# Performance work log

Measured on AMD Instinct MI355X. Metric: run time of the kernel, lower is better.

Reference implementation:

```python
import jax, jax.numpy as jnp
import numpy as np

B, S, D, H = 2, 1024, 768, 12
HD = D // H          # head_dim = 64
DFF = 4 * D          # 3072
EPS = 1e-5


def _ln(x, g, b):
    m = x.mean(-1, keepdims=True)
    v = ((x - m) ** 2).mean(-1, keepdims=True)
    return (x - m) * jax.lax.rsqrt(v + EPS) * g + b


def setup_inputs() -> dict:
    key = jax.random.key(0)
    ks = jax.random.split(key, 8)
    w = lambda k, shape: jax.random.normal(k, shape, jnp.float32) * 0.02
    return {
        "inp": jax.random.normal(ks[0], (B, S, D), jnp.float32),
        "attention_mask": jnp.zeros((B, S), bool),  # True = masked out (filled with -inf)
        "rel_matrix": jax.random.randint(ks[1], (B, S, S), -1, 2, jnp.int32),  # values in {-1,0,1}
        "qkv_w": w(ks[2], (3 * D, D)),
        "rel_A": w(ks[3], (3, HD)),        # relative_position_emb_A.weight
        "o_w": w(ks[4], (D, D)),
        "w1": w(ks[5], (DFF, D)), "b1": jnp.zeros((DFF,), jnp.float32),
        "w2": w(ks[6], (D, DFF)), "b2": jnp.zeros((D,), jnp.float32),
        "ln1_g": jnp.ones((D,), jnp.float32), "ln1_b": jnp.zeros((D,), jnp.float32),
        "ln2_g": jnp.ones((D,), jnp.float32), "ln2_b": jnp.zeros((D,), jnp.float32),
    }


def reference(inp, attention_mask, rel_matrix, qkv_w, rel_A, o_w,
              w1, b1, w2, b2, ln1_g, ln1_b, ln2_g, ln2_b):
    x = _ln(inp, ln1_g, ln1_b)
    qkv = x @ qkv_w.T                                  # (B,S,3D)
    q, k, v = jnp.split(qkv, 3, axis=-1)
    heads = lambda t: t.reshape(B, S, H, HD).transpose(0, 2, 1, 3)  # (B,H,S,HD)
    q, k, v = heads(q), heads(k), heads(v)

    # q @ (k + rel_emb)^T without materializing k_aug:
    # q.k^T term plus per-(q,key) relative term gathered from q @ A^T.
    logits = jnp.einsum("bhqd,bhkd->bhqk", q, k)       # (B,H,S,S)
    r = jnp.einsum("bhqd,cd->bhqc", q, rel_A)          # (B,H,S,3)
    idx = (rel_matrix + 1).astype(jnp.int32)           # (B,S,S) in {0,1,2}
    rel = jnp.take_along_axis(r, jnp.broadcast_to(idx[:, None], (B, H, S, S)), axis=-1)
    logits = (logits + rel) / np.sqrt(HD).astype(np.float32)
    # masked_fill: -inf where mask is True
    logits = jnp.where(attention_mask[:, None, None, :], -jnp.inf, logits)

    attn = jax.nn.softmax(logits, axis=-1)
    out = jnp.einsum("bhqk,bhkd->bhqd", attn, v)
    out = out.transpose(0, 2, 1, 3).reshape(B, S, D)
    inp = inp + out @ o_w.T                            # residual (dropout=0)

    h = _ln(inp, ln2_g, ln2_b)
    mlp = jax.nn.relu(h @ w1.T + b1) @ w2.T + b2
    return inp + mlp
```

## Files before the change

kernel.cpp:

```cpp
#include <hip/hip_runtime.h>
#include <hip/hip_bf16.h>

#define BB 2
#define SS 1024
#define DD 768
#define HH 12
#define HD 64
#define DFF 3072
#define EPS 1e-5f
#define BS2 (BB * SS)
#define BSD ((size_t)BS2 * DD)

typedef unsigned short ushort_t;
typedef unsigned char uchar_t;
using short8 = __attribute__((ext_vector_type(8))) short;
using f32x4  = __attribute__((ext_vector_type(4))) float;

__device__ __forceinline__ ushort_t f2bf_rne(float f) {
    union { float f; unsigned u; } x; x.f = f;
    unsigned r = x.u + 0x7fff + ((x.u >> 16) & 1);
    return (ushort_t)(r >> 16);
}
__device__ __forceinline__ float bf2f(short u) {
    union { unsigned i; float f; } x;
    x.i = ((unsigned)(ushort_t)u) << 16;
    return x.f;
}

#define CVT_N1 (3 * DD * DD / 4)
#define CVT_N2 (CVT_N1 + DD * DD / 4)
#define CVT_N3 (CVT_N2 + DFF * DD / 4)
#define CVT_NT (CVT_N3 + DD * DFF / 4)
#define PREP_CVT   (CVT_NT / 256)
#define PREP_CODES (BB * SS)
#define PREP_LN    BS2

__global__ __launch_bounds__(256) void prep_kernel(
    const float* __restrict__ qkv_w, const float* __restrict__ o_w,
    const float* __restrict__ w1, const float* __restrict__ w2,
    ushort_t* __restrict__ wdst,
    const int* __restrict__ rel, const uchar_t* __restrict__ mask,
    unsigned* __restrict__ codes,
    const float* __restrict__ x, const float* __restrict__ g,
    const float* __restrict__ b, ushort_t* __restrict__ y)
{
    const int bx = blockIdx.x;
    const int t  = threadIdx.x;
    if (bx < PREP_CVT) {
        int i = bx * 256 + t;
        const float* src; int off;
        if (i < CVT_N1)      { src = qkv_w; off = i; }
        else if (i < CVT_N2) { src = o_w;   off = i - CVT_N1; }
        else if (i < CVT_N3) { src = w1;    off = i - CVT_N2; }
        else                 { src = w2;    off = i - CVT_N3; }
        float4 v = ((const float4*)src)[off];
        ushort4 o;
        o.x = f2bf_rne(v.x); o.y = f2bf_rne(v.y);
        o.z = f2bf_rne(v.z); o.w = f2bf_rne(v.w);
        ((ushort4*)wdst)[i] = o;
        return;
    }
    if (bx < PREP_CVT + PREP_CODES) {
        int tid = (bx - PREP_CVT) * 256 + t;
        int l15 = tid & 15;
        int kt  = (tid >> 4) & 15;
        int q   = (tid >> 8) & (SS - 1);
        int bb  = tid >> 18;
        const int* rrow = rel + ((size_t)(bb * SS + q)) * SS + kt * 64 + l15;
        const uchar_t* mrow = mask + (size_t)bb * SS + kt * 64 + l15;
        unsigned o = 0;
#pragma unroll
        for (int nt = 0; nt < 4; ++nt) {
            unsigned c = mrow[nt * 16] ? 3u : (unsigned)(rrow[nt * 16] + 1);
            o |= c << (8 * nt);
        }
        codes[((size_t)(bb * SS + q) * 16 + kt) * 16 + l15] = o;
        return;
    }
    const int row = bx - PREP_CVT - PREP_CODES;
    const float* xr = x + (size_t)row * DD;
    float s = 0.f, ss = 0.f;
    for (int i = t; i < DD; i += 256) {
        float v = xr[i];
        s += v; ss += v * v;
    }
    for (int off = 32; off; off >>= 1) {
        s  += __shfl_down(s,  off);
        ss += __shfl_down(ss, off);
    }
    __shared__ float reds[4], redss[4], bc[2];
    if ((t & 63) == 0) { reds[t >> 6] = s; redss[t >> 6] = ss; }
    __syncthreads();
    if (t == 0) {
        float S1 = reds[0] + reds[1] + reds[2] + reds[3];
        float S2 = redss[0] + redss[1] + redss[2] + redss[3];
        float mean = S1 / DD;
        float var = S2 / DD - mean * mean;
        bc[0] = mean;
        bc[1] = rsqrtf(var + EPS);
    }
    __syncthreads();
    float mean = bc[0], inv = bc[1];
    ushort_t* yr = y + (size_t)row * DD;
    for (int i = t; i < DD; i += 256) {
        yr[i] = f2bf_rne((xr[i] - mean) * inv * g[i] + b[i]);
    }
}

__global__ __launch_bounds__(256) void merge2_ln_kernel(
    const float* __restrict__ part, const float* __restrict__ inp,
    const float* __restrict__ g, const float* __restrict__ b,
    float* __restrict__ resid, ushort_t* __restrict__ h_bf)
{
    const int row = blockIdx.x;
    const int t = threadIdx.x;
    float4 v = make_float4(0.f, 0.f, 0.f, 0.f);
    const size_t idx = (size_t)row * (DD / 4) + t;
    if (t < DD / 4) {
        v = ((const float4*)inp)[idx];
        float4 p0 = ((const float4*)part)[idx];
        float4 p1 = ((const float4*)(part + BSD))[idx];
        v.x += p0.x + p1.x; v.y += p0.y + p1.y;
        v.z += p0.z + p1.z; v.w += p0.w + p1.w;
        ((float4*)resid)[idx] = v;
    }
    float s  = v.x + v.y + v.z + v.w;
    float ss = v.x * v.x + v.y * v.y + v.z * v.z + v.w * v.w;
    for (int off = 32; off; off >>= 1) {
        s  += __shfl_down(s,  off);
        ss += __shfl_down(ss, off);
    }
    __shared__ float reds[4], redss[4], bc[2];
    if ((t & 63) == 0) { reds[t >> 6] = s; redss[t >> 6] = ss; }
    __syncthreads();
    if (t == 0) {
        float S1 = reds[0] + reds[1] + reds[2] + reds[3];
        float S2 = redss[0] + redss[1] + redss[2] + redss[3];
        float mean = S1 / DD;
        float var = S2 / DD - mean * mean;
        bc[0] = mean;
        bc[1] = rsqrtf(var + EPS);
    }
    __syncthreads();
    if (t < DD / 4) {
        const float mean = bc[0], inv = bc[1];
        float4 gv = ((const float4*)g)[t];
        float4 bv = ((const float4*)b)[t];
        ushort4 o;
        o.x = f2bf_rne((v.x - mean) * inv * gv.x + bv.x);
        o.y = f2bf_rne((v.y - mean) * inv * gv.y + bv.y);
        o.z = f2bf_rne((v.z - mean) * inv * gv.z + bv.z);
        o.w = f2bf_rne((v.w - mean) * inv * gv.w + bv.w);
        ((ushort4*)h_bf)[idx] = o;
    }
}

__global__ __launch_bounds__(256) void merge4_kernel(
    const float* __restrict__ part, const float* __restrict__ resid,
    const float* __restrict__ b2, float* __restrict__ outp, int n4)
{
    int i = blockIdx.x * 256 + threadIdx.x;
    if (i >= n4) return;
    float4 v = ((const float4*)resid)[i];
    int col4 = (i * 4) % DD;
    float4 bv = *(const float4*)(b2 + col4);
    v.x += bv.x; v.y += bv.y; v.z += bv.z; v.w += bv.w;
#pragma unroll
    for (int z = 0; z < 4; ++z) {
        float4 pz = ((const float4*)(part + (size_t)z * BSD))[i];
        v.x += pz.x; v.y += pz.y; v.z += pz.z; v.w += pz.w;
    }
    ((float4*)outp)[i] = v;
}

template <bool RELU, bool OUT_BF16, bool HAS_BIAS, bool PARTIAL>
__global__ __launch_bounds__(256) void gemm_tile(
    const ushort_t* __restrict__ A, const ushort_t* __restrict__ W,
    const float* __restrict__ bias, void* __restrict__ Cout,
    int M, int N, int K, int Ksplit)
{
    __shared__ __align__(16) ushort_t As[512 * 8];
    __shared__ __align__(16) ushort_t Bs[1024 * 8];

    const int t  = threadIdx.x;
    const int n0 = blockIdx.x * 128;
    const int m0 = blockIdx.y * 64;
    const int kb = blockIdx.z * Ksplit;
    const int w  = t >> 6;
    const int l  = t & 63;
    const int wm = (w & 1) * 32;
    const int wn = (w >> 1) * 64;
    const int l15  = l & 15;
    const int quad = l >> 4;

    const ushort_t* gA = A + (size_t)(m0 + (t & 63)) * K + kb + (t >> 6) * 8;
    ushort_t* lA = &As[(size_t)t * 8];
    const ushort_t* gB = W + (size_t)(n0 + (t & 127)) * K + kb + (t >> 7) * 8;
    ushort_t* lB = &Bs[(size_t)t * 8];

    f32x4 acc[2][4] = {};

    for (int k0 = 0; k0 < Ksplit; k0 += 64) {
        __syncthreads();
        __builtin_amdgcn_global_load_lds(
            (const __attribute__((address_space(1))) unsigned int*)(gA + k0),
            (__attribute__((address_space(3))) unsigned int*)lA, 16, 0, 0);
        __builtin_amdgcn_global_load_lds(
            (const __attribute__((address_space(1))) unsigned int*)(gA + k0 + 32),
            (__attribute__((address_space(3))) unsigned int*)(lA + 256 * 8), 16, 0, 0);
#pragma unroll
        for (int ii = 0; ii < 4; ++ii)
            __builtin_amdgcn_global_load_lds(
                (const __attribute__((address_space(1))) unsigned int*)(gB + k0 + ii * 16),
                (__attribute__((address_space(3))) unsigned int*)(lB + (size_t)ii * 256 * 8),
                16, 0, 0);
        __syncthreads();

#pragma unroll
        for (int ks = 0; ks < 2; ++ks) {
            const ushort_t* aptr = &As[(size_t)((ks * 4 + quad) * 64 + wm + l15) * 8];
            const ushort_t* bptr = &Bs[(size_t)((ks * 4 + quad) * 128 + wn + l15) * 8];
            short8 af[2], bf[4];
#pragma unroll
            for (int i = 0; i < 2; ++i)
                af[i] = *(const short8*)(aptr + (size_t)i * 16 * 8);
#pragma unroll
            for (int j = 0; j < 4; ++j)
                bf[j] = *(const short8*)(bptr + (size_t)j * 16 * 8);
#pragma unroll
            for (int i = 0; i < 2; ++i)
#pragma unroll
                for (int j = 0; j < 4; ++j)
                    acc[i][j] = __builtin_amdgcn_mfma_f32_16x16x32_bf16(
                        af[i], bf[j], acc[i][j], 0, 0, 0);
        }
    }

    if (PARTIAL) {
        float* Cp = (float*)Cout + (size_t)blockIdx.z * ((size_t)M * N);
#pragma unroll
        for (int i = 0; i < 2; ++i) {
            const int row = m0 + wm + i * 16 + quad * 4;
#pragma unroll
            for (int j = 0; j < 4; ++j) {
                const int col = n0 + wn + j * 16 + l15;
#pragma unroll
                for (int r = 0; r < 4; ++r)
                    Cp[(size_t)(row + r) * N + col] = acc[i][j][r];
            }
        }
    } else {
#pragma unroll
        for (int i = 0; i < 2; ++i) {
            const int row = m0 + wm + i * 16 + quad * 4;
#pragma unroll
            for (int j = 0; j < 4; ++j) {
                const int col = n0 + wn + j * 16 + l15;
                const float bv = HAS_BIAS ? bias[col] : 0.f;
#pragma unroll
                for (int r = 0; r < 4; ++r) {
                    float v = acc[i][j][r] + bv;
                    if (RELU) v = fmaxf(v, 0.f);
                    if (OUT_BF16)
                        ((ushort_t*)Cout)[(size_t)(row + r) * N + col] = f2bf_rne(v);
                    else
                        ((float*)Cout)[(size_t)(row + r) * N + col] = v;
                }
            }
        }
    }
}

__global__ __launch_bounds__(256) void attn_mfma_kernel(
    const ushort_t* __restrict__ qkv,
    const unsigned* __restrict__ codes,
    const float* __restrict__ rel_A,
    ushort_t* __restrict__ Opart,
    float* __restrict__ lpart)
{
    __shared__ __align__(16) ushort_t Ks[64 * 64];
    __shared__ __align__(16) unsigned Vt2[64 * 36];
    __shared__ __align__(16) ushort_t Ps[64 * 72];
    __shared__ __align__(16) float r3s[64][4];

    const int bx = blockIdx.x;
    const int ks = bx & 1;
    const int qt = (bx >> 1) & 15;
    const int h  = (bx >> 5) % HH;
    const int b  = bx / (32 * HH);
    const int q0 = qt * 64;
    const int t  = threadIdx.x;
    const int w  = t >> 6;
    const int l  = t & 63;
    const int l15  = l & 15;
    const int quad = l >> 4;

    const size_t qrow = (size_t)(b * SS + q0 + w * 16 + l15) * (3 * DD) + h * HD;
    const short8 qf0 = *(const short8*)(qkv + qrow + quad * 8);
    const short8 qf1 = *(const short8*)(qkv + qrow + 32 + quad * 8);

    {
        float rv[3];
#pragma unroll
        for (int c = 0; c < 3; ++c) {
            const float* a = rel_A + c * HD + quad * 8;
            float acc = 0.f;
#pragma unroll
            for (int j = 0; j < 8; ++j) acc += bf2f(qf0[j]) * a[j];
#pragma unroll
            for (int j = 0; j < 8; ++j) acc += bf2f(qf1[j]) * a[32 + j];
            acc += __shfl_xor(acc, 16);
            acc += __shfl_xor(acc, 32);
            rv[c] = acc;
        }
        if (quad == 0) {
            float4 f4 = make_float4(rv[0], rv[1], rv[2], -2.4e31f);
            *(float4*)&r3s[w * 16 + l15][0] = f4;
        }
    }
    __syncthreads();
    float4 r3v[4];
#pragma unroll
    for (int reg = 0; reg < 4; ++reg)
        r3v[reg] = *(const float4*)&r3s[w * 16 + quad * 4 + reg][0];

    float l_run[4] = {0.f, 0.f, 0.f, 0.f};
    f32x4 oacc[4] = {};

    for (int kt = ks * 8; kt < ks * 8 + 8; ++kt) {
        const int k0 = kt * 64;
        __syncthreads();
        {
            const int r  = t >> 3;
            const int cp = t & 7;
            const int cl  = cp ^ (r & 7);
            const ushort_t* g = qkv + (size_t)(b * SS + k0 + r) * (3 * DD) + DD + h * HD + cl * 8;
            __builtin_amdgcn_global_load_lds(
                (const __attribute__((address_space(1))) unsigned*)g,
                (__attribute__((address_space(3))) unsigned*)(Ks + (size_t)t * 8), 16, 0, 0);
            const int r2  = r + 32;
            const int cl2 = cp ^ (r2 & 7);
            const ushort_t* g2 = qkv + (size_t)(b * SS + k0 + r2) * (3 * DD) + DD + h * HD + cl2 * 8;
            __builtin_amdgcn_global_load_lds(
                (const __attribute__((address_space(1))) unsigned*)g2,
                (__attribute__((address_space(3))) unsigned*)(Ks + (size_t)(t + 256) * 8), 16, 0, 0);
        }
        {
            const int kp = t >> 3;
            const int dg = t & 7;
            const ushort_t* g = qkv + (size_t)(b * SS + k0 + 2 * kp) * (3 * DD) + 2 * DD + h * HD + dg * 8;
            short8 va = *(const short8*)g;
            short8 vb = *(const short8*)(g + 3 * DD);
            const int kps = kp ^ ((dg & 7) * 4);
#pragma unroll
            for (int i = 0; i < 8; ++i)
                Vt2[(size_t)(dg * 8 + i) * 36 + kps] =
                    (unsigned)(ushort_t)va[i] | ((unsigned)(ushort_t)vb[i] << 16);
        }
        __syncthreads();

        f32x4 sacc[4] = {};
#pragma unroll
        for (int kc = 0; kc < 2; ++kc) {
            const short8 qv = kc ? qf1 : qf0;
#pragma unroll
            for (int nt = 0; nt < 4; ++nt) {
                const int row = nt * 16 + l15;
                const int cp  = (kc * 4 + quad) ^ (row & 7);
                const short8 kf = *(const short8*)(Ks + (size_t)row * 64 + cp * 8);
                sacc[nt] = __builtin_amdgcn_mfma_f32_16x16x32_bf16(qv, kf, sacc[nt], 0, 0, 0);
            }
        }

#pragma unroll
        for (int reg = 0; reg < 4; ++reg) {
            const int qloc = w * 16 + quad * 4 + reg;
            const unsigned cds = codes[((size_t)(b * SS + q0 + qloc) * 16 + kt) * 16 + l15];
            const float4 r4 = r3v[reg];
#pragma unroll
            for (int nt = 0; nt < 4; ++nt) {
                const unsigned c = (cds >> (8 * nt)) & 0xff;
                float rvv = (c == 0) ? r4.x : (c == 1) ? r4.y : (c == 2) ? r4.z : r4.w;
                const float p = __expf((sacc[nt][reg] + rvv) * 0.125f);
                l_run[reg] += p;
                Ps[(size_t)qloc * 72 + nt * 16 + l15] = f2bf_rne(p);
            }
        }

#pragma unroll
        for (int kc = 0; kc < 2; ++kc) {
            const short8 pf = *(const short8*)(Ps + (size_t)(w * 16 + l15) * 72 + kc * 32 + quad * 8);
#pragma unroll
            for (int dt = 0; dt < 4; ++dt) {
                const int d  = dt * 16 + l15;
                const int dg = d >> 3;
                const int kps0 = (kc * 16 + quad * 4) ^ ((dg & 7) * 4);
                const short8 vf = *(const short8*)((const ushort_t*)&Vt2[(size_t)d * 36 + kps0]);
                oacc[dt] = __builtin_amdgcn_mfma_f32_16x16x32_bf16(pf, vf, oacc[dt], 0, 0, 0);
            }
        }
    }

    ushort_t* Op = Opart + (size_t)ks * BSD;
    float* lp = lpart + (size_t)ks * BS2 * HH;
#pragma unroll
    for (int reg = 0; reg < 4; ++reg) {
        float ls = l_run[reg];
        ls += __shfl_xor(ls, 1);
        ls += __shfl_xor(ls, 2);
        ls += __shfl_xor(ls, 4);
        ls += __shfl_xor(ls, 8);
        const int orow = b * SS + q0 + w * 16 + quad * 4 + reg;
#pragma unroll
        for (int dt = 0; dt < 4; ++dt)
            Op[(size_t)orow * DD + h * HD + dt * 16 + l15] = f2bf_rne(oacc[dt][reg]);
        if (l15 == 0) lp[(size_t)orow * HH + h] = ls;
    }
}

__global__ __launch_bounds__(256) void attn_merge(
    const ushort_t* __restrict__ Opart, const float* __restrict__ lpart,
    ushort_t* __restrict__ att_bf)
{
    int i = blockIdx.x * 256 + threadIdx.x;
    int row = (i * 4) / DD;
    int h   = ((i * 4) % DD) >> 6;
    float l0 = lpart[(size_t)row * HH + h];
    float l1 = lpart[(size_t)BS2 * HH + (size_t)row * HH + h];
    float inv = 1.0f / (l0 + l1);
    ushort4 a = ((const ushort4*)Opart)[i];
    ushort4 b = ((const ushort4*)(Opart + BSD))[i];
    ushort4 o;
    o.x = f2bf_rne((bf2f(a.x) + bf2f(b.x)) * inv);
    o.y = f2bf_rne((bf2f(a.y) + bf2f(b.y)) * inv);
    o.z = f2bf_rne((bf2f(a.z) + bf2f(b.z)) * inv);
    o.w = f2bf_rne((bf2f(a.w) + bf2f(b.w)) * inv);
    ((ushort4*)att_bf)[i] = o;
}

extern "C" void kernel_launch(void* const* d_in, const int* in_sizes, int n_in,
                              void* d_out, int out_size, void* d_ws, size_t ws_size,
                              hipStream_t stream) {
    const float* inp   = (const float*)d_in[0];
    const uchar_t* amask = (const uchar_t*)d_in[1];
    const int*   relm  = (const int*)d_in[2];
    const float* qkv_w = (const float*)d_in[3];
    const float* rel_A = (const float*)d_in[4];
    const float* o_w   = (const float*)d_in[5];
    const float* w1    = (const float*)d_in[6];
    const float* b1    = (const float*)d_in[7];
    const float* w2    = (const float*)d_in[8];
    const float* b2    = (const float*)d_in[9];
    const float* ln1_g = (const float*)d_in[10];
    const float* ln1_b = (const float*)d_in[11];
    const float* ln2_g = (const float*)d_in[12];
    const float* ln2_b = (const float*)d_in[13];
    float* out = (float*)d_out;

    char* p = (char*)d_ws;
    ushort_t* x_bf   = (ushort_t*)p; p += BSD * 2;
    ushort_t* att_bf = (ushort_t*)p; p += BSD * 2;
    ushort_t* h_bf   = (ushort_t*)p; p += BSD * 2;
    ushort_t* ff_bf  = (ushort_t*)p; p += (size_t)BS2 * DFF * 2;
    ushort_t* qkvw_bf= (ushort_t*)p; p += (size_t)3 * DD * DD * 2;
    ushort_t* ow_bf  = (ushort_t*)p; p += (size_t)DD * DD * 2;
    ushort_t* w1_bf  = (ushort_t*)p; p += (size_t)DFF * DD * 2;
    ushort_t* w2_bf  = (ushort_t*)p; p += (size_t)DD * DFF * 2;
    ushort_t* qkv_bf = (ushort_t*)p; p += (size_t)BS2 * 3 * DD * 2;
    float*    resid  = (float*)p;    p += BSD * 4;
    float*    pool   = (float*)p;    p += 4 * BSD * 4;
    ushort_t* Opart  = (ushort_t*)p; p += 2 * BSD * 2;
    float*    lpart  = (float*)p;    p += (size_t)2 * BS2 * HH * 4;
    unsigned* codes  = (unsigned*)p; p += (size_t)BB * SS * SS;

    prep_kernel<<<PREP_CVT + PREP_CODES + PREP_LN, 256, 0, stream>>>(
        qkv_w, o_w, w1, w2, qkvw_bf, relm, amask, codes,
        inp, ln1_g, ln1_b, x_bf);

    gemm_tile<false, true, false, false>
        <<<dim3(3 * DD / 128, BS2 / 64, 1), 256, 0, stream>>>(
        x_bf, qkvw_bf, nullptr, qkv_bf, BS2, 3 * DD, DD, DD);

    attn_mfma_kernel<<<BB * HH * 16 * 2, 256, 0, stream>>>(
        qkv_bf, codes, rel_A, Opart, lpart);
    attn_merge<<<(int)(BSD / 4 / 256), 256, 0, stream>>>(Opart, lpart, att_bf);

    gemm_tile<false, false, false, true>
        <<<dim3(DD / 128, BS2 / 64, 2), 256, 0, stream>>>(
        att_bf, ow_bf, nullptr, pool, BS2, DD, DD, DD / 2);

    merge2_ln_kernel<<<BS2, 256, 0, stream>>>(
        pool, inp, ln2_g, ln2_b, resid, h_bf);

    gemm_tile<true, true, true, false>
        <<<dim3(DFF / 128, BS2 / 64, 1), 256, 0, stream>>>(
        h_bf, w1_bf, b1, ff_bf, BS2, DFF, DD, DD);

    gemm_tile<false, false, false, true>
        <<<dim3(DD / 128, BS2 / 64, 4), 256, 0, stream>>>(
        ff_bf, w2_bf, nullptr, pool, BS2, DD, DFF, DFF / 4);

    merge4_kernel<<<(int)(BSD / 4 / 256), 256, 0, stream>>>(
        pool, resid, b2, out, (int)(BSD / 4));
}
```

Baseline: 266.9 us.

## Double-buffer GEMM and attention LDS tiles; store split-K partials as bf16

New measurement: 265.8 us. No clear change (-0.4%).

```diff
diff --git a/kernel.cpp b/kernel.cpp
--- a/kernel.cpp
+++ b/kernel.cpp
@@ -108,7 +108,7 @@
 }
 
 __global__ __launch_bounds__(256) void merge2_ln_kernel(
-    const float* __restrict__ part, const float* __restrict__ inp,
+    const ushort_t* __restrict__ part, const float* __restrict__ inp,
     const float* __restrict__ g, const float* __restrict__ b,
     float* __restrict__ resid, ushort_t* __restrict__ h_bf)
 {
@@ -118,10 +118,12 @@
     const size_t idx = (size_t)row * (DD / 4) + t;
     if (t < DD / 4) {
         v = ((const float4*)inp)[idx];
-        float4 p0 = ((const float4*)part)[idx];
-        float4 p1 = ((const float4*)(part + BSD))[idx];
-        v.x += p0.x + p1.x; v.y += p0.y + p1.y;
-        v.z += p0.z + p1.z; v.w += p0.w + p1.w;
+        ushort4 p0 = ((const ushort4*)part)[idx];
+        ushort4 p1 = ((const ushort4*)(part + BSD))[idx];
+        v.x += bf2f(p0.x) + bf2f(p1.x);
+        v.y += bf2f(p0.y) + bf2f(p1.y);
+        v.z += bf2f(p0.z) + bf2f(p1.z);
+        v.w += bf2f(p0.w) + bf2f(p1.w);
         ((float4*)resid)[idx] = v;
     }
     float s  = v.x + v.y + v.z + v.w;
@@ -156,7 +158,7 @@
 }
 
 __global__ __launch_bounds__(256) void merge4_kernel(
-    const float* __restrict__ part, const float* __restrict__ resid,
+    const ushort_t* __restrict__ part, const float* __restrict__ resid,
     const float* __restrict__ b2, float* __restrict__ outp, int n4)
 {
     int i = blockIdx.x * 256 + threadIdx.x;
@@ -167,8 +169,9 @@
     v.x += bv.x; v.y += bv.y; v.z += bv.z; v.w += bv.w;
 #pragma unroll
     for (int z = 0; z < 4; ++z) {
-        float4 pz = ((const float4*)(part + (size_t)z * BSD))[i];
-        v.x += pz.x; v.y += pz.y; v.z += pz.z; v.w += pz.w;
+        ushort4 pz = ((const ushort4*)(part + (size_t)z * BSD))[i];
+        v.x += bf2f(pz.x); v.y += bf2f(pz.y);
+        v.z += bf2f(pz.z); v.w += bf2f(pz.w);
     }
     ((float4*)outp)[i] = v;
 }
@@ -179,8 +182,8 @@
     const float* __restrict__ bias, void* __restrict__ Cout,
     int M, int N, int K, int Ksplit)
 {
-    __shared__ __align__(16) ushort_t As[512 * 8];
-    __shared__ __align__(16) ushort_t Bs[1024 * 8];
+    __shared__ __align__(16) ushort_t As[2][512 * 8];
+    __shared__ __align__(16) ushort_t Bs[2][1024 * 8];
 
     const int t  = threadIdx.x;
     const int n0 = blockIdx.x * 128;
@@ -194,32 +197,53 @@
     const int quad = l >> 4;
 
     const ushort_t* gA = A + (size_t)(m0 + (t & 63)) * K + kb + (t >> 6) * 8;
-    ushort_t* lA = &As[(size_t)t * 8];
     const ushort_t* gB = W + (size_t)(n0 + (t & 127)) * K + kb + (t >> 7) * 8;
-    ushort_t* lB = &Bs[(size_t)t * 8];
 
     f32x4 acc[2][4] = {};
 
-    for (int k0 = 0; k0 < Ksplit; k0 += 64) {
-        __syncthreads();
+    {
+        ushort_t* lA = &As[0][(size_t)t * 8];
+        ushort_t* lB = &Bs[0][(size_t)t * 8];
         __builtin_amdgcn_global_load_lds(
-            (const __attribute__((address_space(1))) unsigned int*)(gA + k0),
+            (const __attribute__((address_space(1))) unsigned int*)(gA),
             (__attribute__((address_space(3))) unsigned int*)lA, 16, 0, 0);
         __builtin_amdgcn_global_load_lds(
-            (const __attribute__((address_space(1))) unsigned int*)(gA + k0 + 32),
+            (const __attribute__((address_space(1))) unsigned int*)(gA + 32),
             (__attribute__((address_space(3))) unsigned int*)(lA + 256 * 8), 16, 0, 0);
 #pragma unroll
         for (int ii = 0; ii < 4; ++ii)
             __builtin_amdgcn_global_load_lds(
-                (const __attribute__((address_space(1))) unsigned int*)(gB + k0 + ii * 16),
+                (const __attribute__((address_space(1))) unsigned int*)(gB + ii * 16),
                 (__attribute__((address_space(3))) unsigned int*)(lB + (size_t)ii * 256 * 8),
                 16, 0, 0);
+    }
+
+    const int nIter = Ksplit >> 6;
+    for (int it = 0; it < nIter; ++it) {
         __syncthreads();
-
+        if (it + 1 < nIter) {
+            const int k0 = (it + 1) << 6;
+            const int nb = (it + 1) & 1;
+            ushort_t* lA = &As[nb][(size_t)t * 8];
+            ushort_t* lB = &Bs[nb][(size_t)t * 8];
+            __builtin_amdgcn_global_load_lds(
+                (const __attribute__((address_space(1))) unsigned int*)(gA + k0),
+                (__attribute__((address_space(3))) unsigned int*)lA, 16, 0, 0);
+            __builtin_amdgcn_global_load_lds(
+                (const __attribute__((address_space(1))) unsigned int*)(gA + k0 + 32),
+                (__attribute__((address_space(3))) unsigned int*)(lA + 256 * 8), 16, 0, 0);
+#pragma unroll
+            for (int ii = 0; ii < 4; ++ii)
+                __builtin_amdgcn_global_load_lds(
+                    (const __attribute__((address_space(1))) unsigned int*)(gB + k0 + ii * 16),
+                    (__attribute__((address_space(3))) unsigned int*)(lB + (size_t)ii * 256 * 8),
+                    16, 0, 0);
+        }
+        const int buf = it & 1;
 #pragma unroll
         for (int ks = 0; ks < 2; ++ks) {
-            const ushort_t* aptr = &As[(size_t)((ks * 4 + quad) * 64 + wm + l15) * 8];
-            const ushort_t* bptr = &Bs[(size_t)((ks * 4 + quad) * 128 + wn + l15) * 8];
+            const ushort_t* aptr = &As[buf][(size_t)((ks * 4 + quad) * 64 + wm + l15) * 8];
+            const ushort_t* bptr = &Bs[buf][(size_t)((ks * 4 + quad) * 128 + wn + l15) * 8];
             short8 af[2], bf[4];
 #pragma unroll
             for (int i = 0; i < 2; ++i)
@@ -237,7 +261,7 @@
     }
 
     if (PARTIAL) {
-        float* Cp = (float*)Cout + (size_t)blockIdx.z * ((size_t)M * N);
+        ushort_t* Cp = (ushort_t*)Cout + (size_t)blockIdx.z * ((size_t)M * N);
 #pragma unroll
         for (int i = 0; i < 2; ++i) {
             const int row = m0 + wm + i * 16 + quad * 4;
@@ -246,7 +270,7 @@
                 const int col = n0 + wn + j * 16 + l15;
 #pragma unroll
                 for (int r = 0; r < 4; ++r)
-                    Cp[(size_t)(row + r) * N + col] = acc[i][j][r];
+                    Cp[(size_t)(row + r) * N + col] = f2bf_rne(acc[i][j][r]);
             }
         }
     } else {
@@ -278,8 +302,8 @@
     ushort_t* __restrict__ Opart,
     float* __restrict__ lpart)
 {
-    __shared__ __align__(16) ushort_t Ks[64 * 64];
-    __shared__ __align__(16) unsigned Vt2[64 * 36];
+    __shared__ __align__(16) ushort_t Ks[2][64 * 64];
+    __shared__ __align__(16) unsigned Vt2[2][64 * 36];
     __shared__ __align__(16) ushort_t Ps[64 * 72];
     __shared__ __align__(16) float r3s[64][4];
 
@@ -295,6 +319,12 @@
     const int l15  = l & 15;
     const int quad = l >> 4;
 
+    const int sr  = t >> 3;
+    const int scp = t & 7;
+    const int vkp = t >> 3;
+    const int vdg = t & 7;
+    const int vkps = vkp ^ (vdg * 4);
+
     const size_t qrow = (size_t)(b * SS + q0 + w * 16 + l15) * (3 * DD) + h * HD;
     const short8 qf0 = *(const short8*)(qkv + qrow + quad * 8);
     const short8 qf1 = *(const short8*)(qkv + qrow + 32 + quad * 8);
@@ -318,46 +348,61 @@
             *(float4*)&r3s[w * 16 + l15][0] = f4;
         }
     }
+
+    float l_run[4] = {0.f, 0.f, 0.f, 0.f};
+    f32x4 oacc[4] = {};
+
+    const int kt0 = ks * 8;
+    short8 va, vb;
+    {
+        const int k0 = kt0 * 64;
+        const int cl  = scp ^ (sr & 7);
+        const ushort_t* g = qkv + (size_t)(b * SS + k0 + sr) * (3 * DD) + DD + h * HD + cl * 8;
+        __builtin_amdgcn_global_load_lds(
+            (const __attribute__((address_space(1))) unsigned*)g,
+            (__attribute__((address_space(3))) unsigned*)(&Ks[0][0] + (size_t)t * 8), 16, 0, 0);
+        const int r2  = sr + 32;
+        const int cl2 = scp ^ (r2 & 7);
+        const ushort_t* g2 = qkv + (size_t)(b * SS + k0 + r2) * (3 * DD) + DD + h * HD + cl2 * 8;
+        __builtin_amdgcn_global_load_lds(
+            (const __attribute__((address_space(1))) unsigned*)g2,
+            (__attribute__((address_space(3))) unsigned*)(&Ks[0][0] + (size_t)(t + 256) * 8), 16, 0, 0);
+        const ushort_t* gv = qkv + (size_t)(b * SS + k0 + 2 * vkp) * (3 * DD) + 2 * DD + h * HD + vdg * 8;
+        va = *(const short8*)gv;
+        vb = *(const short8*)(gv + 3 * DD);
+#pragma unroll
+        for (int i = 0; i < 8; ++i)
+            Vt2[0][(size_t)(vdg * 8 + i) * 36 + vkps] =
+                (unsigned)(ushort_t)va[i] | ((unsigned)(ushort_t)vb[i] << 16);
+    }
     __syncthreads();
     float4 r3v[4];
 #pragma unroll
     for (int reg = 0; reg < 4; ++reg)
         r3v[reg] = *(const float4*)&r3s[w * 16 + quad * 4 + reg][0];
 
-    float l_run[4] = {0.f, 0.f, 0.f, 0.f};
-    f32x4 oacc[4] = {};
-
-    for (int kt = ks * 8; kt < ks * 8 + 8; ++kt) {
-        const int k0 = kt * 64;
-        __syncthreads();
-        {
-            const int r  = t >> 3;
-            const int cp = t & 7;
-            const int cl  = cp ^ (r & 7);
-            const ushort_t* g = qkv + (size_t)(b * SS + k0 + r) * (3 * DD) + DD + h * HD + cl * 8;
+    for (int i8 = 0; i8 < 8; ++i8) {
+        const int kt  = kt0 + i8;
+        const int cur = i8 & 1;
+        const bool more = (i8 + 1 < 8);
+        if (more) {
+            const int k0 = (kt + 1) * 64;
+            const int nb = cur ^ 1;
+            const int cl  = scp ^ (sr & 7);
+            const ushort_t* g = qkv + (size_t)(b * SS + k0 + sr) * (3 * DD) + DD + h * HD + cl * 8;
             __builtin_amdgcn_global_load_lds(
                 (const __attribute__((address_space(1))) unsigned*)g,
-                (__attribute__((address_space(3))) unsigned*)(Ks + (size_t)t * 8), 16, 0, 0);
-            const int r2  = r + 32;
-            const int cl2 = cp ^ (r2 & 7);
+                (__attribute__((address_space(3))) unsigned*)(&Ks[nb][0] + (size_t)t * 8), 16, 0, 0);
+            const int r2  = sr + 32;
+            const int cl2 = scp ^ (r2 & 7);
             const ushort_t* g2 = qkv + (size_t)(b * SS + k0 + r2) * (3 * DD) + DD + h * HD + cl2 * 8;
             __builtin_amdgcn_global_load_lds(
                 (const __attribute__((address_space(1))) unsigned*)g2,
-                (__attribute__((address_space(3))) unsigned*)(Ks + (size_t)(t + 256) * 8), 16, 0, 0);
-        }
-        {
-            const int kp = t >> 3;
-            const int dg = t & 7;
-            const ushort_t* g = qkv + (size_t)(b * SS + k0 + 2 * kp) * (3 * DD) + 2 * DD + h * HD + dg * 8;
-            short8 va = *(const short8*)g;
-            short8 vb = *(const short8*)(g + 3 * DD);
-            const int kps = kp ^ ((dg & 7) * 4);
-#pragma unroll
-            for (int i = 0; i < 8; ++i)
-                Vt2[(size_t)(dg * 8 + i) * 36 + kps] =
-                    (unsigned)(ushort_t)va[i] | ((unsigned)(ushort_t)vb[i] << 16);
-        }
-        __syncthreads();
+                (__attribute__((address_space(3))) unsigned*)(&Ks[nb][0] + (size_t)(t + 256) * 8), 16, 0, 0);
+            const ushort_t* gv = qkv + (size_t)(b * SS + k0 + 2 * vkp) * (3 * DD) + 2 * DD + h * HD + vdg * 8;
+            va = *(const short8*)gv;
+            vb = *(const short8*)(gv + 3 * DD);
+        }
 
         f32x4 sacc[4] = {};
 #pragma unroll
@@ -367,7 +412,7 @@
             for (int nt = 0; nt < 4; ++nt) {
                 const int row = nt * 16 + l15;
                 const int cp  = (kc * 4 + quad) ^ (row & 7);
-                const short8 kf = *(const short8*)(Ks + (size_t)row * 64 + cp * 8);
+                const short8 kf = *(const short8*)(&Ks[cur][0] + (size_t)row * 64 + cp * 8);
                 sacc[nt] = __builtin_amdgcn_mfma_f32_16x16x32_bf16(qv, kf, sacc[nt], 0, 0, 0);
             }
         }
@@ -395,9 +440,18 @@
                 const int d  = dt * 16 + l15;
                 const int dg = d >> 3;
                 const int kps0 = (kc * 16 + quad * 4) ^ ((dg & 7) * 4);
-                const short8 vf = *(const short8*)((const ushort_t*)&Vt2[(size_t)d * 36 + kps0]);
+                const short8 vf = *(const short8*)((const ushort_t*)&Vt2[cur][(size_t)d * 36 + kps0]);
                 oacc[dt] = __builtin_amdgcn_mfma_f32_16x16x32_bf16(pf, vf, oacc[dt], 0, 0, 0);
             }
+        }
+
+        if (more) {
+            const int nb = cur ^ 1;
+#pragma unroll
+            for (int i = 0; i < 8; ++i)
+                Vt2[nb][(size_t)(vdg * 8 + i) * 36 + vkps] =
+                    (unsigned)(ushort_t)va[i] | ((unsigned)(ushort_t)vb[i] << 16);
+            __syncthreads();
         }
     }
 
@@ -468,7 +522,7 @@
     ushort_t* w2_bf  = (ushort_t*)p; p += (size_t)DD * DFF * 2;
     ushort_t* qkv_bf = (ushort_t*)p; p += (size_t)BS2 * 3 * DD * 2;
     float*    resid  = (float*)p;    p += BSD * 4;
-    float*    pool   = (float*)p;    p += 4 * BSD * 4;
+    ushort_t* pool   = (ushort_t*)p; p += 4 * BSD * 2;
     ushort_t* Opart  = (ushort_t*)p; p += 2 * BSD * 2;
     float*    lpart  = (float*)p;    p += (size_t)2 * BS2 * HH * 4;
     unsigned* codes  = (unsigned*)p; p += (size_t)BB * SS * SS;
```
